# Performance work log

Hardware: AMD Instinct MI355X
Metric: run time of the kernel (lower is better)

The kernel has to match this reference:

```python
import jax, jax.numpy as jnp
import numpy as np

LN_EPS = 1e-5
LOG_EPS = 1e-8

def _layernorm(x, w, b):
    mu = jnp.mean(x, axis=-1, keepdims=True)
    var = jnp.mean((x - mu) ** 2, axis=-1, keepdims=True)
    return (x - mu) * jax.lax.rsqrt(var + LN_EPS) * w + b


def setup_inputs() -> dict:
    key = jax.random.key(0)
    ks = jax.random.split(key, 8)
    B, T, D = 4, 4096, 1024
    x = jax.random.normal(ks[0], (B, T, D), dtype=jnp.float32)
    ln_w = jnp.ones((D,), jnp.float32)
    ln_b = jnp.zeros((D,), jnp.float32)
    # torch Linear stores weight as (out, in)
    Wf = jax.random.normal(ks[1], (D, D), jnp.float32) / np.sqrt(D)
    bf = jax.random.normal(ks[2], (D,), jnp.float32) * 0.02
    # module inits reach to zeros; use small random values for a non-trivial baseline
    Wr = jax.random.normal(ks[3], (D, D), jnp.float32) * 0.02
    br = jax.random.normal(ks[4], (D,), jnp.float32) * 0.02
    alpha_bias = jnp.array([3.0], jnp.float32) + jax.random.normal(ks[5], (1,), jnp.float32) * 0.1
    beta_scale = jnp.array([0.02], jnp.float32)
    return {"x": x, "ln_w": ln_w, "ln_b": ln_b, "Wf": Wf, "bf": bf,
            "Wr": Wr, "br": br, "alpha_bias": alpha_bias, "beta_scale": beta_scale}


def reference(x, ln_w, ln_b, Wf, bf, Wr, br, alpha_bias, beta_scale):
    residual = x
    x_norm = _layernorm(x, ln_w, ln_b)                       # [B,T,D]
    alpha = jax.nn.sigmoid(jnp.einsum('btd,ed->bte', x_norm, Wf) + bf + alpha_bias)
    beta_x = beta_scale * (1.0 - alpha) * x_norm
    log_alpha = jnp.log(alpha + LOG_EPS)
    log_alpha_cumsum = jnp.cumsum(log_alpha, axis=1)          # [B,T,D]
    m = jnp.max(log_alpha_cumsum, axis=1, keepdims=True)      # [B,1,D]
    scale = jnp.exp(log_alpha_cumsum - m)
    x_star = beta_x * scale
    s_star = jnp.cumsum(x_star, axis=1)
    output = s_star / (scale + LOG_EPS)
    x_gate = jnp.tanh(jnp.einsum('btd,ed->bte', output, Wr) + br)
    return x_gate * 0.05 + residual
```

## Files before the change

### kernel.cpp

```cpp
#include <hip/hip_runtime.h>

#define D_DIM 1024
#define B_DIM 4
#define T_DIM 4096
#define M_DIM (B_DIM * T_DIM)
#define CHUNK 32
#define NCHUNK (T_DIM / CHUNK)
#define NWAVE_C 16
#define SEG (NCHUNK / NWAVE_C)
#define NKT (D_DIM / 32)

typedef unsigned short u16;
typedef __attribute__((ext_vector_type(8))) __bf16 bf16x8;
typedef __attribute__((ext_vector_type(4))) float f32x4;

__device__ __forceinline__ float bf2f(u16 u) {
    union { unsigned int i; float f; } v;
    v.i = ((unsigned int)u) << 16;
    return v.f;
}
__device__ __forceinline__ u16 f2bf(float f) {
    union { float f; unsigned int i; } v;
    v.f = f;
    unsigned int u = v.i;
    unsigned int r = (u + 0x7fffu + ((u >> 16) & 1u)) >> 16;
    return (u16)r;
}
__device__ __forceinline__ float fast_tanh(float v) {
    float e = __expf(2.f * v);
    return 1.f - 2.f / (e + 1.f);
}

#define GLOAD16(g, l)                                                   \
    __builtin_amdgcn_global_load_lds(                                   \
        (const __attribute__((address_space(1))) void*)(g),             \
        (__attribute__((address_space(3))) void*)(l), 16, 0, 0)

#define BAR()                                      \
    do {                                           \
        asm volatile("" ::: "memory");             \
        __builtin_amdgcn_s_barrier();              \
        asm volatile("" ::: "memory");             \
    } while (0)

#define WAITVM(N) asm volatile("s_waitcnt vmcnt(" #N ")" ::: "memory")

__global__ __launch_bounds__(256) void ln_conv_kernel(const float* __restrict__ x,
                                                      const float* __restrict__ w,
                                                      const float* __restrict__ b,
                                                      u16* __restrict__ xn,
                                                      const float* __restrict__ Wf,
                                                      const float* __restrict__ Wr,
                                                      u16* __restrict__ da,
                                                      u16* __restrict__ db) {
    int tid = threadIdx.x;
    if (blockIdx.x < 2048) {
        int i = blockIdx.x * 256 + tid;
        const float* s = (i < 262144) ? Wf : Wr;
        u16* dp = (i < 262144) ? da : db;
        int j = i & 262143;
        float4 v = ((const float4*)s)[j];
        ushort4 o;
        o.x = f2bf(v.x); o.y = f2bf(v.y); o.z = f2bf(v.z); o.w = f2bf(v.w);
        ((ushort4*)dp)[j] = o;
        return;
    }
    int wv = tid >> 6, lane = tid & 63;
    int row = (blockIdx.x - 2048) * 4 + wv;
    const float4* xr = (const float4*)(x + (size_t)row * D_DIM);
    float4 xv[4];
    #pragma unroll
    for (int k = 0; k < 4; k++) xv[k] = xr[lane + 64 * k];
    float s = 0.f, s2 = 0.f;
    #pragma unroll
    for (int k = 0; k < 4; k++) {
        s  += xv[k].x + xv[k].y + xv[k].z + xv[k].w;
        s2 += xv[k].x * xv[k].x + xv[k].y * xv[k].y
            + xv[k].z * xv[k].z + xv[k].w * xv[k].w;
    }
    #pragma unroll
    for (int o = 1; o < 64; o <<= 1) {
        s  += __shfl_xor(s, o, 64);
        s2 += __shfl_xor(s2, o, 64);
    }
    float mu = s * (1.0f / D_DIM);
    float var = s2 * (1.0f / D_DIM) - mu * mu;
    float rs = rsqrtf(var + 1e-5f);
    ushort4* xo = (ushort4*)(xn + (size_t)row * D_DIM);
    #pragma unroll
    for (int k = 0; k < 4; k++) {
        float4 wv4 = ((const float4*)w)[lane + 64 * k];
        float4 bv4 = ((const float4*)b)[lane + 64 * k];
        ushort4 o;
        o.x = f2bf((xv[k].x - mu) * rs * wv4.x + bv4.x);
        o.y = f2bf((xv[k].y - mu) * rs * wv4.y + bv4.y);
        o.z = f2bf((xv[k].z - mu) * rs * wv4.z + bv4.z);
        o.w = f2bf((xv[k].w - mu) * rs * wv4.w + bv4.w);
        xo[lane + 64 * k] = o;
    }
}

__device__ __forceinline__ void gemm256_core(const u16* __restrict__ AG,
                                             const u16* __restrict__ BG,
                                             int tile_m, int tile_n,
                                             u16* ldsA, u16* ldsB,
                                             f32x4 (*acc)[4]) {
    int tid  = threadIdx.x;
    int wave = tid >> 6, lane = tid & 63;
    int wr = wave >> 2, wc = wave & 3;
    int lrow = lane >> 2;
    int sswz = (lane & 3) ^ (lrow & 3);
    const u16* gA = AG + (size_t)(tile_m + wave * 32 + lrow) * D_DIM + sswz * 8;
    const u16* gB = BG + (size_t)(tile_n + wave * 32 + lrow) * D_DIM + sswz * 8;
    int ldst = wave * 1024 + lane * 8;
    int fr = lane & 15, q = lane >> 4;
    int sw = (q ^ (lane & 3)) * 8;
    const u16* pAb = ldsA + (wr * 128 + fr) * 32 + sw;
    const u16* pBb = ldsB + (wc * 64 + fr) * 32 + sw;

#define STG(ldsb, gsrc, tt)                                                  \
    do {                                                                     \
        GLOAD16((gsrc) + (size_t)(tt) * 32,                                  \
                (ldsb) + ((tt) & 3) * 8192 + ldst);                          \
        GLOAD16((gsrc) + (size_t)(tt) * 32 + (size_t)16 * D_DIM,             \
                (ldsb) + ((tt) & 3) * 8192 + 512 + ldst);                    \
    } while (0)

    STG(ldsA, gA, 0); STG(ldsB, gB, 0);
    STG(ldsA, gA, 1); STG(ldsB, gB, 1);
    STG(ldsA, gA, 2); STG(ldsB, gB, 2);
    WAITVM(8);
    BAR();

    for (int t = 0; t < NKT; t++) {
        const int c = t & 3;
        const u16* pA = pAb + c * 8192;
        const u16* pB = pBb + c * 8192;
        bf16x8 Af[8], Bf[4];
        #pragma unroll
        for (int ni = 0; ni < 4; ni++) Bf[ni] = *(const bf16x8*)(pB + ni * 512);
        #pragma unroll
        for (int mi = 0; mi < 8; mi++) Af[mi] = *(const bf16x8*)(pA + mi * 512);
        #pragma unroll
        for (int mi = 0; mi < 8; mi++)
            #pragma unroll
            for (int ni = 0; ni < 4; ni++)
                acc[mi][ni] = __builtin_amdgcn_mfma_f32_16x16x32_bf16(
                    Af[mi], Bf[ni], acc[mi][ni], 0, 0, 0);
        if (t + 3 < NKT) {
            STG(ldsA, gA, t + 3);
            STG(ldsB, gB, t + 3);
            WAITVM(8);
        } else if (t + 2 < NKT) {
            WAITVM(4);
        } else if (t + 1 < NKT) {
            WAITVM(0);
        }
        BAR();
    }
#undef STG
}

__global__ __launch_bounds__(512, 2) void gemm1_kernel(const u16* __restrict__ xn,
                                                       const u16* __restrict__ Wfc,
                                                       const float* __restrict__ bf_,
                                                       const float* __restrict__ ab,
                                                       const float* __restrict__ bs,
                                                       u16* __restrict__ out_la,
                                                       float* __restrict__ Sg,
                                                       float* __restrict__ Tg) {
    __shared__ __align__(16) u16 lds[65536];
    u16* ldsA = lds;
    u16* ldsB = lds + 32768;
    int flat = blockIdx.y * 4 + blockIdx.x;
    int xcd = flat & 7, p = flat >> 3;
    int tile_m = (xcd * 8 + (p >> 2)) * 256;
    int tile_n = (p & 3) * 256;
    f32x4 acc[8][4] = {};
    gemm256_core(xn, Wfc, tile_m, tile_n, ldsA, ldsB, acc);

    int tid = threadIdx.x, wave = tid >> 6, lane = tid & 63;
    int wr = wave >> 2, wc = wave & 3;
    int q = lane >> 4, l = lane & 15;
    #pragma unroll
    for (int j = 0; j < 16; j++) {
        int xrow = wave * 32 + j * 2 + (lane >> 5);
        int xslot = (lane & 31) ^ (xrow & 3);
        GLOAD16(xn + (size_t)(tile_m + xrow) * D_DIM + tile_n + xslot * 8,
                lds + wave * 8192 + j * 512 + lane * 8);
    }
    WAITVM(0);
    BAR();

    float abv = ab[0], bsv = bs[0];
    #pragma unroll
    for (int ni = 0; ni < 4; ni++) {
        int col = tile_n + wc * 64 + ni * 16 + l;
        float bcol = bf_[col];
        #pragma unroll
        for (int ch = 0; ch < 4; ch++) {
            float lav[2][4], bxv[2][4];
            #pragma unroll
            for (int h = 0; h < 2; h++) {
                int mi = 2 * ch + h;
                #pragma unroll
                for (int r = 0; r < 4; r++) {
                    int rl = wr * 128 + mi * 16 + q * 4 + r;
                    int cl = wc * 64 + ni * 16 + l;
                    int row = tile_m + rl;
                    float z = acc[mi][ni][r] + bcol + abv;
                    float alpha = 1.f / (1.f + __expf(-z));
                    float la_ = __logf(alpha + 1e-8f);
                    float xv = bf2f(lds[rl * 256 + (((cl >> 3) ^ (rl & 3)) * 8) + (cl & 7)]);
                    lav[h][r] = la_;
                    bxv[h][r] = bsv * (1.f - alpha) * xv;
                    out_la[(size_t)row * D_DIM + col] = f2bf(la_);
                }
            }
            float s0 = lav[0][0] + lav[0][1] + lav[0][2] + lav[0][3];
            float s1 = lav[1][0] + lav[1][1] + lav[1][2] + lav[1][3];
            float x0 = s0, x1 = s1, y;
            y = __shfl_up(x0, 16, 64); if (q >= 1) x0 += y;
            y = __shfl_up(x0, 32, 64); if (q >= 2) x0 += y;
            y = __shfl_up(x1, 16, 64); if (q >= 1) x1 += y;
            y = __shfl_up(x1, 32, 64); if (q >= 2) x1 += y;
            float t0 = __shfl(x0, l + 48, 64);
            float t1 = __shfl(x1, l + 48, 64);
            float e0 = x0 - s0, e1 = x1 - s1;
            float pr = e0, Tp = 0.f;
            #pragma unroll
            for (int r = 0; r < 4; r++) { pr += lav[0][r]; Tp += bxv[0][r] * __expf(pr); }
            pr = t0 + e1;
            #pragma unroll
            for (int r = 0; r < 4; r++) { pr += lav[1][r]; Tp += bxv[1][r] * __expf(pr); }
            Tp += __shfl_xor(Tp, 16, 64);
            Tp += __shfl_xor(Tp, 32, 64);
            if (q == 0) {
                int cidx = ((tile_m + wr * 128) >> 5) + ch;
                Sg[(size_t)cidx * D_DIM + col] = t0 + t1;
                Tg[(size_t)cidx * D_DIM + col] = Tp;
            }
        }
    }
}

__global__ __launch_bounds__(1024) void scan_combine(const u16* __restrict__ la,
                                                     const float* __restrict__ S,
                                                     const float* __restrict__ Tb,
                                                     float* __restrict__ Of,
                                                     float* __restrict__ SSp) {
    __shared__ float lsS[NWAVE_C][64], lsW[NWAVE_C][64];
    int b = blockIdx.x >> 4;
    int dg = blockIdx.x & 15;
    int wave = threadIdx.x >> 6, lane = threadIdx.x & 63;
    int d = dg * 64 + lane;
    float m = bf2f(la[(size_t)(b * T_DIM) * D_DIM + d]);
    size_t base = ((size_t)b * NCHUNK) * D_DIM + d;
    int c0 = wave * SEG;

    float OfR[SEG], wR[SEG];
    float Or = 0.f, w = 0.f;
    #pragma unroll
    for (int j = 0; j < SEG; j++) {
        size_t ci = base + (size_t)(c0 + j) * D_DIM;
        OfR[j] = Or;
        wR[j]  = w;
        w  += __expf(Or) * Tb[ci];
        Or += S[ci];
    }
    lsS[wave][lane] = Or; lsW[wave][lane] = w;
    __syncthreads();

    float o = 0.f, s = 0.f, myO = 0.f, myS = 0.f;
    #pragma unroll
    for (int w2 = 0; w2 < NWAVE_C; w2++) {
        if (w2 == wave) { myO = o; myS = s; }
        s += __expf(o - m) * lsW[w2][lane];
        o += lsS[w2][lane];
    }

    float em = __expf(myO - m);
    #pragma unroll
    for (int j = 0; j < SEG; j++) {
        size_t ci = base + (size_t)(c0 + j) * D_DIM;
        Of[ci]  = myO + OfR[j] - m;
        SSp[ci] = myS + em * wR[j];
    }
}

__global__ __launch_bounds__(256) void scan_final(const u16* __restrict__ la,
                                                  const u16* __restrict__ xn,
                                                  const float* __restrict__ bs,
                                                  const float* __restrict__ Of,
                                                  const float* __restrict__ SSp,
                                                  u16* __restrict__ osc) {
    int bc = blockIdx.x;
    int b = bc >> 7, c = bc & (NCHUNK - 1);
    int col0 = threadIdx.x * 4;
    float bsv = bs[0];
    size_t base = ((size_t)(b * T_DIM + c * CHUNK)) * D_DIM + col0;
    size_t ci = ((size_t)(b * NCHUNK + c)) * D_DIM + col0;
    float ofs[4], ss[4], p[4];
    #pragma unroll
    for (int j = 0; j < 4; j++) { ofs[j] = Of[ci + j]; ss[j] = SSp[ci + j]; p[j] = 0.f; }
    #pragma unroll 8
    for (int t = 0; t < CHUNK; t++) {
        size_t idx = base + (size_t)t * D_DIM;
        ushort4 lv = *(const ushort4*)(la + idx);
        ushort4 xv = *(const ushort4*)(xn + idx);
        u16 lvs[4] = {lv.x, lv.y, lv.z, lv.w};
        u16 xvs[4] = {xv.x, xv.y, xv.z, xv.w};
        u16 os[4];
        #pragma unroll
        for (int j = 0; j < 4; j++) {
            float lav = bf2f(lvs[j]);
            p[j] += lav;
            float scv = __expf(ofs[j] + p[j]);
            float bx = bsv * (1.f - __expf(lav)) * bf2f(xvs[j]);
            ss[j] += bx * scv;
            os[j] = f2bf(ss[j] / (scv + 1e-8f));
        }
        ushort4 o; o.x = os[0]; o.y = os[1]; o.z = os[2]; o.w = os[3];
        *(ushort4*)(osc + idx) = o;
    }
}

__global__ __launch_bounds__(512, 2) void gemm2_kernel(const u16* __restrict__ A,
                                                       const u16* __restrict__ Bm,
                                                       const float* __restrict__ bias,
                                                       const float* __restrict__ resid,
                                                       float* __restrict__ out_f) {
    __shared__ __align__(16) u16 lds[65536];
    u16* ldsA = lds;
    u16* ldsB = lds + 32768;
    int flat = blockIdx.y * 4 + blockIdx.x;
    int xcd = flat & 7, p = flat >> 3;
    int tile_m = (xcd * 8 + (p >> 2)) * 256;
    int tile_n = (p & 3) * 256;
    f32x4 acc[8][4] = {};
    gemm256_core(A, Bm, tile_m, tile_n, ldsA, ldsB, acc);

    int tid = threadIdx.x, wave = tid >> 6, lane = tid & 63;
    int wr = wave >> 2, wc = wave & 3;
    int q = lane >> 4, l = lane & 15;
    #pragma unroll
    for (int mi = 0; mi < 8; mi++) {
        #pragma unroll
        for (int r = 0; r < 4; r++) {
            int row = tile_m + wr * 128 + mi * 16 + q * 4 + r;
            #pragma unroll
            for (int ni = 0; ni < 4; ni++) {
                int col = tile_n + wc * 64 + ni * 16 + l;
                size_t idx = (size_t)row * D_DIM + col;
                float g = fast_tanh(acc[mi][ni][r] + bias[col]);
                out_f[idx] = 0.05f * g + resid[idx];
            }
        }
    }
}

extern "C" void kernel_launch(void* const* d_in, const int* in_sizes, int n_in,
                              void* d_out, int out_size, void* d_ws, size_t ws_size,
                              hipStream_t stream) {
    const float* x   = (const float*)d_in[0];
    const float* lnw = (const float*)d_in[1];
    const float* lnb = (const float*)d_in[2];
    const float* Wf  = (const float*)d_in[3];
    const float* bf_ = (const float*)d_in[4];
    const float* Wr  = (const float*)d_in[5];
    const float* br  = (const float*)d_in[6];
    const float* ab  = (const float*)d_in[7];
    const float* bs  = (const float*)d_in[8];
    float* out = (float*)d_out;

    char* w = (char*)d_ws;
    u16* xn  = (u16*)w;
    u16* la  = (u16*)(w + (size_t)33554432);
    u16* Wfc = (u16*)(w + (size_t)67108864);
    u16* Wrc = (u16*)(w + (size_t)69206016);
    float* S   = (float*)(w + (size_t)71303168);
    float* Tb  = S  + 524288;
    float* Of  = Tb + 524288;
    float* SSp = Of + 524288;
    u16* osc = xn;

    ln_conv_kernel<<<dim3(2048 + M_DIM / 4), dim3(256), 0, stream>>>(
        x, lnw, lnb, xn, Wf, Wr, Wfc, Wrc);
    gemm1_kernel<<<dim3(D_DIM / 256, M_DIM / 256), dim3(512), 0, stream>>>(
        xn, Wfc, bf_, ab, bs, la, S, Tb);
    scan_combine<<<dim3(B_DIM * 16), dim3(1024), 0, stream>>>(la, S, Tb, Of, SSp);
    scan_final<<<dim3(B_DIM * NCHUNK), dim3(256), 0, stream>>>(la, xn, bs, Of, SSp, osc);
    gemm2_kernel<<<dim3(D_DIM / 256, M_DIM / 256), dim3(512), 0, stream>>>(
        osc, Wrc, br, x, out);
}
```

Before: 268.6 us.

## Load GEMM B fragments directly from global into registers, bypassing LDS

The shared GEMM core no longer stages the weight (B) tile through LDS. Each wave now loads its B fragments straight from global memory into registers, prefetching one k-step ahead, while A stays in the 4-stage LDS ring. This halves the LDS footprint and removes the B staging traffic and LDS reads. In exchange, each wave re-fetches B redundantly from global/L2 (waves sharing a column repeat the load), and the vmcnt waits now also cover the B loads.

```diff
diff --git a/kernel.cpp b/kernel.cpp
--- a/kernel.cpp
+++ b/kernel.cpp
@@ -103,7 +103,7 @@
 __device__ __forceinline__ void gemm256_core(const u16* __restrict__ AG,
                                              const u16* __restrict__ BG,
                                              int tile_m, int tile_n,
-                                             u16* ldsA, u16* ldsB,
+                                             u16* ldsA,
                                              f32x4 (*acc)[4]) {
     int tid  = threadIdx.x;
     int wave = tid >> 6, lane = tid & 63;
@@ -111,34 +111,38 @@
     int lrow = lane >> 2;
     int sswz = (lane & 3) ^ (lrow & 3);
     const u16* gA = AG + (size_t)(tile_m + wave * 32 + lrow) * D_DIM + sswz * 8;
-    const u16* gB = BG + (size_t)(tile_n + wave * 32 + lrow) * D_DIM + sswz * 8;
     int ldst = wave * 1024 + lane * 8;
     int fr = lane & 15, q = lane >> 4;
     int sw = (q ^ (lane & 3)) * 8;
     const u16* pAb = ldsA + (wr * 128 + fr) * 32 + sw;
-    const u16* pBb = ldsB + (wc * 64 + fr) * 32 + sw;
-
-#define STG(ldsb, gsrc, tt)                                                  \
+    const u16* pBF[4];
+    #pragma unroll
+    for (int ni = 0; ni < 4; ni++)
+        pBF[ni] = BG + (size_t)(tile_n + wc * 64 + ni * 16 + fr) * D_DIM + q * 8;
+
+#define STGA(tt)                                                             \
     do {                                                                     \
-        GLOAD16((gsrc) + (size_t)(tt) * 32,                                  \
-                (ldsb) + ((tt) & 3) * 8192 + ldst);                          \
-        GLOAD16((gsrc) + (size_t)(tt) * 32 + (size_t)16 * D_DIM,             \
-                (ldsb) + ((tt) & 3) * 8192 + 512 + ldst);                    \
+        GLOAD16(gA + (size_t)(tt) * 32,                                      \
+                ldsA + ((tt) & 3) * 8192 + ldst);                            \
+        GLOAD16(gA + (size_t)(tt) * 32 + (size_t)16 * D_DIM,                 \
+                ldsA + ((tt) & 3) * 8192 + 512 + ldst);                      \
     } while (0)
 
-    STG(ldsA, gA, 0); STG(ldsB, gB, 0);
-    STG(ldsA, gA, 1); STG(ldsB, gB, 1);
-    STG(ldsA, gA, 2); STG(ldsB, gB, 2);
+    STGA(0); STGA(1); STGA(2);
+    bf16x8 Bcur[4], Bnxt[4];
+    #pragma unroll
+    for (int ni = 0; ni < 4; ni++) Bcur[ni] = *(const bf16x8*)(pBF[ni]);
     WAITVM(8);
     BAR();
 
     for (int t = 0; t < NKT; t++) {
-        const int c = t & 3;
-        const u16* pA = pAb + c * 8192;
-        const u16* pB = pBb + c * 8192;
-        bf16x8 Af[8], Bf[4];
-        #pragma unroll
-        for (int ni = 0; ni < 4; ni++) Bf[ni] = *(const bf16x8*)(pB + ni * 512);
+        if (t + 1 < NKT) {
+            #pragma unroll
+            for (int ni = 0; ni < 4; ni++)
+                Bnxt[ni] = *(const bf16x8*)(pBF[ni] + (size_t)(t + 1) * 32);
+        }
+        const u16* pA = pAb + (t & 3) * 8192;
+        bf16x8 Af[8];
         #pragma unroll
         for (int mi = 0; mi < 8; mi++) Af[mi] = *(const bf16x8*)(pA + mi * 512);
         #pragma unroll
@@ -146,19 +150,18 @@
             #pragma unroll
             for (int ni = 0; ni < 4; ni++)
                 acc[mi][ni] = __builtin_amdgcn_mfma_f32_16x16x32_bf16(
-                    Af[mi], Bf[ni], acc[mi][ni], 0, 0, 0);
+                    Af[mi], Bcur[ni], acc[mi][ni], 0, 0, 0);
+        #pragma unroll
+        for (int ni = 0; ni < 4; ni++) Bcur[ni] = Bnxt[ni];
         if (t + 3 < NKT) {
-            STG(ldsA, gA, t + 3);
-            STG(ldsB, gB, t + 3);
-            WAITVM(8);
-        } else if (t + 2 < NKT) {
+            STGA(t + 3);
+            WAITVM(12);
+        } else {
             WAITVM(4);
-        } else if (t + 1 < NKT) {
-            WAITVM(0);
         }
         BAR();
     }
-#undef STG
+#undef STGA
 }
 
 __global__ __launch_bounds__(512, 2) void gemm1_kernel(const u16* __restrict__ xn,
@@ -170,14 +173,12 @@
                                                        float* __restrict__ Sg,
                                                        float* __restrict__ Tg) {
     __shared__ __align__(16) u16 lds[65536];
-    u16* ldsA = lds;
-    u16* ldsB = lds + 32768;
     int flat = blockIdx.y * 4 + blockIdx.x;
     int xcd = flat & 7, p = flat >> 3;
     int tile_m = (xcd * 8 + (p >> 2)) * 256;
     int tile_n = (p & 3) * 256;
     f32x4 acc[8][4] = {};
-    gemm256_core(xn, Wfc, tile_m, tile_n, ldsA, ldsB, acc);
+    gemm256_core(xn, Wfc, tile_m, tile_n, lds, acc);
 
     int tid = threadIdx.x, wave = tid >> 6, lane = tid & 63;
     int wr = wave >> 2, wc = wave & 3;
@@ -330,15 +331,13 @@
                                                        const float* __restrict__ bias,
                                                        const float* __restrict__ resid,
                                                        float* __restrict__ out_f) {
-    __shared__ __align__(16) u16 lds[65536];
-    u16* ldsA = lds;
-    u16* ldsB = lds + 32768;
+    __shared__ __align__(16) u16 lds[32768];
     int flat = blockIdx.y * 4 + blockIdx.x;
     int xcd = flat & 7, p = flat >> 3;
     int tile_m = (xcd * 8 + (p >> 2)) * 256;
     int tile_n = (p & 3) * 256;
     f32x4 acc[8][4] = {};
-    gemm256_core(A, Bm, tile_m, tile_n, ldsA, ldsB, acc);
+    gemm256_core(A, Bm, tile_m, tile_n, lds, acc);
 
     int tid = threadIdx.x, wave = tid >> 6, lane = tid & 63;
     int wr = wave >> 2, wc = wave & 3;
```

Result: slower. 283.2 us (+5.4%).
